# Kernel optimization log

Hardware: AMD Instinct MI355X
Metric: run time of the kernel (lower is better)

## Reference

```python
import jax, jax.numpy as jnp
import numpy as np

N_NODES = 50000
N_EDGES = 800000
DIM = 256
HEADS = 8
DIM_OUT = 32  # per-head; dim_inner = HEADS*DIM_OUT = 256


def setup_inputs() -> dict:
    key = jax.random.key(0)
    ks = jax.random.split(key, 9)
    s = 1.0 / np.sqrt(DIM)
    inner = HEADS * DIM_OUT
    return {
        "x": jax.random.normal(ks[0], (N_NODES, DIM), dtype=jnp.float32),
        "Wq": jax.random.uniform(ks[1], (DIM, inner), jnp.float32, -s, s),
        "bq": jax.random.uniform(ks[2], (inner,), jnp.float32, -s, s),
        "Wk": jax.random.uniform(ks[3], (DIM, inner), jnp.float32, -s, s),
        "bk": jax.random.uniform(ks[4], (inner,), jnp.float32, -s, s),
        "Wv": jax.random.uniform(ks[5], (DIM, inner), jnp.float32, -s, s),
        "bv": jax.random.uniform(ks[6], (inner,), jnp.float32, -s, s),
        "src": jax.random.randint(ks[7], (N_EDGES,), 0, N_NODES),
        "dst": jax.random.randint(ks[8], (N_EDGES,), 0, N_NODES),
    }


def reference(x, Wq, bq, Wk, bk, Wv, bv, src, dst):
    n = x.shape[0]
    q = (x @ Wq + bq).reshape(n, HEADS, DIM_OUT)
    k = (x @ Wk + bk).reshape(n, HEADS, DIM_OUT)
    v = (x @ Wv + bv).reshape(n, HEADS, DIM_OUT)
    # edge-wise u_dot_v: dot of src query with dst key, per head -> [E, H]
    scores = jnp.einsum('ehd,ehd->eh', q[src], k[dst]) / jnp.sqrt(
        jnp.asarray(DIM_OUT, dtype=x.dtype))
    # segment softmax over incoming edges of each destination node
    m = jax.ops.segment_max(scores, dst, num_segments=n)  # [N, H]
    m = jnp.where(jnp.isfinite(m), m, 0.0)
    e = jnp.exp(scores - m[dst])
    z = jax.ops.segment_sum(e, dst, num_segments=n)  # [N, H]
    p = e / jnp.maximum(z[dst], 1e-16)  # [E, H]
    # u_mul_e_sum: sum over incoming edges of src values weighted by attn
    out = jax.ops.segment_sum(v[src] * p[:, :, None], dst, num_segments=n)
    return out.reshape(n, HEADS * DIM_OUT)  # concat=True
```

## Files before the change

kernel.cpp:

```cpp
#include <hip/hip_runtime.h>
#include <math.h>

#define N_NODES 50000
#define N_EDGES 800000
#define DIM 256
#define HEADS 8
#define DIM_OUT 32
#define INNER 256
#define M_PAD 50048

typedef __attribute__((ext_vector_type(8))) short bf16x8;
typedef __attribute__((ext_vector_type(4))) float f32x4;
typedef __attribute__((ext_vector_type(2))) float f32x2;

__device__ __forceinline__ unsigned short f2bf(float f) {
    unsigned u = __float_as_uint(f);
    unsigned r = (u + 0x7FFFu + ((u >> 16) & 1u)) >> 16;
    return (unsigned short)r;
}

__device__ __forceinline__ f32x2 up2(unsigned u) {
    f32x2 r;
    r.x = __uint_as_float(u << 16);
    r.y = __uint_as_float(u & 0xFFFF0000u);
    return r;
}
__device__ __forceinline__ void up2x4(uint4 r, f32x2* o) {
    o[0] = up2(r.x); o[1] = up2(r.y); o[2] = up2(r.z); o[3] = up2(r.w);
}

__device__ __forceinline__ void gll16(const void* g, void* l) {
    __builtin_amdgcn_global_load_lds(
        (const __attribute__((address_space(1))) unsigned*)(uintptr_t)g,
        (__attribute__((address_space(3))) unsigned*)(unsigned)(uintptr_t)l,
        16, 0, 0);
}

#define NB_CONVX 6256
#define NB_CONVW 768
#define NB_HIST  3125
__global__ __launch_bounds__(256) void prep(
    const float* __restrict__ x,
    const float* __restrict__ Wq, const float* __restrict__ Wk,
    const float* __restrict__ Wv,
    const int* __restrict__ dst,
    unsigned short* __restrict__ xbf, unsigned short* __restrict__ Wt,
    int* __restrict__ deg)
{
    int b = blockIdx.x;
    if (b < NB_CONVX) {
        size_t i8 = ((size_t)b * 256 + threadIdx.x) * 8;
        unsigned short h[8];
        if (i8 < (size_t)N_NODES * 256) {
            float4 a = *(const float4*)(x + i8);
            float4 c = *(const float4*)(x + i8 + 4);
            h[0]=f2bf(a.x); h[1]=f2bf(a.y); h[2]=f2bf(a.z); h[3]=f2bf(a.w);
            h[4]=f2bf(c.x); h[5]=f2bf(c.y); h[6]=f2bf(c.z); h[7]=f2bf(c.w);
        } else {
            #pragma unroll
            for (int j = 0; j < 8; j++) h[j] = 0;
        }
        uint4 o;
        o.x = (unsigned)h[0] | ((unsigned)h[1] << 16);
        o.y = (unsigned)h[2] | ((unsigned)h[3] << 16);
        o.z = (unsigned)h[4] | ((unsigned)h[5] << 16);
        o.w = (unsigned)h[6] | ((unsigned)h[7] << 16);
        *(uint4*)(xbf + i8) = o;
    } else if (b < NB_CONVX + NB_CONVW) {
        int idx = (b - NB_CONVX) * 256 + threadIdx.x;
        int z = idx >> 16, r = idx & 65535;
        int k = r >> 8, n = r & 255;
        const float* W = (z == 0) ? Wq : (z == 1) ? Wk : Wv;
        Wt[(size_t)z * 65536 + n * 256 + k] = f2bf(W[k * 256 + n]);
    } else {
        int e = (b - NB_CONVX - NB_CONVW) * 256 + threadIdx.x;
        if (e < N_EDGES) atomicAdd(deg + dst[e], 1);
    }
}

#define GEMM_NWG 2346
__global__ __launch_bounds__(256) void gemm_qkv(
    const unsigned short* __restrict__ xbf,
    const unsigned short* __restrict__ Wt,
    const float* __restrict__ bq, const float* __restrict__ bk,
    const float* __restrict__ bv,
    unsigned short* __restrict__ q, unsigned short* __restrict__ k,
    unsigned short* __restrict__ v)
{
    int hw = blockIdx.x;
    int xcd = hw & 7, pos = hw >> 3;
    const int q8 = GEMM_NWG >> 3, r8 = GEMM_NWG & 7;
    int lid = (xcd < r8 ? xcd * (q8 + 1) : r8 * (q8 + 1) + (xcd - r8) * q8) + pos;
    int xx = lid / 6;
    int yz = lid - xx * 6;
    const int row0 = xx * 128;
    const int col0 = (yz & 1) * 128;
    const int z = yz >> 1;

    const int t = threadIdx.x;
    const unsigned short* Wz = Wt + (size_t)z * 65536;
    const float* bias = (z == 0) ? bq : (z == 1) ? bk : bv;
    unsigned short* C = (z == 0) ? q : (z == 1) ? k : v;

    __shared__ __align__(16) short As[128 * 32];
    __shared__ __align__(16) short Bs[128 * 32];

    const int wave = t >> 6;
    const int lane = t & 63;
    const int wm = (wave & 1) * 64;
    const int wn = (wave >> 1) * 64;
    const int lr = lane & 15;
    const int lg = lane >> 4;
    const int srow = lane >> 2;
    const int sch  = lane & 3;

    f32x4 acc[4][4] = {};

    for (int k0 = 0; k0 < 256; k0 += 32) {
        #pragma unroll
        for (int c = 0; c < 2; c++) {
            int seg = wave * 2 + c;
            gll16(xbf + (size_t)(row0 + seg * 16 + srow) * 256 + k0 + sch * 8,
                  As + seg * 512);
        }
        #pragma unroll
        for (int c = 0; c < 2; c++) {
            int seg = wave * 2 + c;
            gll16(Wz + (size_t)(col0 + seg * 16 + srow) * 256 + k0 + sch * 8,
                  Bs + seg * 512);
        }
        __syncthreads();

        bf16x8 af[4], bfr[4];
        #pragma unroll
        for (int mi = 0; mi < 4; mi++)
            af[mi] = *(const bf16x8*)&As[(wm + mi * 16 + lr) * 32 + lg * 8];
        #pragma unroll
        for (int ni = 0; ni < 4; ni++)
            bfr[ni] = *(const bf16x8*)&Bs[(wn + ni * 16 + lr) * 32 + lg * 8];
        #pragma unroll
        for (int mi = 0; mi < 4; mi++)
            #pragma unroll
            for (int ni = 0; ni < 4; ni++)
                acc[mi][ni] = __builtin_amdgcn_mfma_f32_16x16x32_bf16(
                    af[mi], bfr[ni], acc[mi][ni], 0, 0, 0);
        __syncthreads();
    }

    #pragma unroll
    for (int mi = 0; mi < 4; mi++) {
        #pragma unroll
        for (int ni = 0; ni < 4; ni++) {
            int gcol = col0 + wn + ni * 16 + lr;
            float bb = bias[gcol];
            #pragma unroll
            for (int r = 0; r < 4; r++) {
                int grow = row0 + wm + mi * 16 + lg * 4 + r;
                if (grow < N_NODES)
                    C[(size_t)grow * 256 + gcol] = f2bf(acc[mi][ni][r] + bb);
            }
        }
    }
}

__global__ __launch_bounds__(1024) void scan_deg(
    const int* __restrict__ deg, int* __restrict__ rowptr)
{
    __shared__ int wsum[16];
    __shared__ int wpre[16];
    int t = threadIdx.x;
    int wid = t >> 6, ln = t & 63;
    int carry = 0;
    for (int base = 0; base < N_NODES; base += 4096) {
        int i4 = base + t * 4;
        int4 dv = {0, 0, 0, 0};
        if (i4 < N_NODES) dv = *(const int4*)(deg + i4);
        int sum = dv.x + dv.y + dv.z + dv.w;
        int inc = sum;
        #pragma unroll
        for (int off = 1; off < 64; off <<= 1) {
            int u = __shfl_up(inc, off);
            if (ln >= off) inc += u;
        }
        if (ln == 63) wsum[wid] = inc;
        __syncthreads();
        if (wid == 0 && ln < 16) {
            int s = wsum[ln];
            int p = s;
            #pragma unroll
            for (int off = 1; off < 16; off <<= 1) {
                int u = __shfl_up(p, off);
                if (ln >= off) p += u;
            }
            wpre[ln] = p - s;
        }
        __syncthreads();
        if (i4 < N_NODES) {
            int r = carry + wpre[wid] + (inc - sum);
            r += dv.x; rowptr[i4 + 1] = r;
            r += dv.y; rowptr[i4 + 2] = r;
            r += dv.z; rowptr[i4 + 3] = r;
            r += dv.w; rowptr[i4 + 4] = r;
        }
        carry += wpre[15] + wsum[15];
        __syncthreads();
    }
    if (t == 0) rowptr[0] = 0;
}

__global__ __launch_bounds__(256) void csr_scatter(
    const int* __restrict__ src, const int* __restrict__ dst,
    const int* __restrict__ rowptr,
    int* __restrict__ deg, int* __restrict__ edge_src)
{
    int e = blockIdx.x * 256 + threadIdx.x;
    if (e >= N_EDGES) return;
    int d = dst[e];
    int old = atomicSub(deg + d, 1);
    edge_src[rowptr[d] + old - 1] = src[e];
}

__global__ __launch_bounds__(256) void node_attn(
    const unsigned short* __restrict__ qbf,
    const unsigned short* __restrict__ kbf,
    const unsigned short* __restrict__ vbf,
    const int* __restrict__ rowptr, const int* __restrict__ edge_src,
    float* __restrict__ out)
{
    int node = blockIdx.x * 4 + (threadIdx.x >> 6);
    int lane = threadIdx.x & 63;
    if (node >= N_NODES) return;
    const int half = lane >> 5;
    const int l = lane & 31;

    int beg = rowptr[node], end = rowptr[node + 1];
    int deg = end - beg;

    float* op = out + (size_t)node * 256 + l * 8;
    if (deg <= 0) {
        if (half == 0) {
            float4 z4 = {0.f, 0.f, 0.f, 0.f};
            *(float4*)op = z4;
            *(float4*)(op + 4) = z4;
        }
        return;
    }

    f32x2 kf2[4];
    up2x4(*(const uint4*)(kbf + (size_t)node * 256 + l * 8), kf2);

    const unsigned short* qrow = qbf + l * 8;
    const unsigned short* vrow = vbf + l * 8;

    const float SC = 0.17677669529663687f * 1.4426950408889634f;

    int U = (deg + 1) >> 1;
    U = ((U + 2) / 3) * 3;
    U = __builtin_amdgcn_readfirstlane(U);

    const int i0 = beg + half;
    const int last = end - 1;

    int tmp0 = edge_src[min(i0,     last)];
    int tmp1 = edge_src[min(i0 + 2, last)];
    int idC  = edge_src[min(i0 + 4, last)];
    int idA  = edge_src[min(i0 + 6, last)];
    int idB  = 0;
    uint4 qA = *(const uint4*)(qrow + (size_t)tmp0 * 256);
    uint4 vA = *(const uint4*)(vrow + (size_t)tmp0 * 256);
    uint4 qB = *(const uint4*)(qrow + (size_t)tmp1 * 256);
    uint4 vB = *(const uint4*)(vrow + (size_t)tmp1 * 256);
    uint4 qC, vC;

    float m = -1e30f, zsum = 0.0f;
    f32x2 af2[4] = {};

#define BODY(QW, VW, QL, VL, IDL, IDF, P)                                    \
    do {                                                                     \
        size_t off_ = (size_t)(IDL) * 256;                                   \
        QL = *(const uint4*)(qrow + off_);                                   \
        VL = *(const uint4*)(vrow + off_);                                   \
        int vi_ = i0 + 2 * t + 2 * (P);                                      \
        IDF = edge_src[min(vi_ + 8, last)];                                  \
        f32x2 qf_[4], vf_[4];                                                \
        up2x4(QW, qf_);                                                      \
        up2x4(VW, vf_);                                                      \
        f32x2 d_ = qf_[0] * kf2[0];                                          \
        d_ += qf_[1] * kf2[1];                                               \
        d_ += qf_[2] * kf2[2];                                               \
        d_ += qf_[3] * kf2[3];                                               \
        float s_ = d_.x + d_.y;                                              \
        s_ += __shfl_xor(s_, 1);                                             \
        s_ += __shfl_xor(s_, 2);                                             \
        bool ok_ = vi_ < end;                                                \
        float sc_ = ok_ ? s_ * SC : -1e30f;                                  \
        float mn_ = fmaxf(m, sc_);                                           \
        float w_ = exp2f(sc_ - mn_);                                         \
        w_ = ok_ ? w_ : 0.0f;                                                \
        float al_ = exp2f(m - mn_);                                          \
        zsum = zsum * al_ + w_;                                              \
        f32x2 a2_ = {al_, al_}, w2_ = {w_, w_};                              \
        af2[0] = af2[0] * a2_ + vf_[0] * w2_;                                \
        af2[1] = af2[1] * a2_ + vf_[1] * w2_;                                \
        af2[2] = af2[2] * a2_ + vf_[2] * w2_;                                \
        af2[3] = af2[3] * a2_ + vf_[3] * w2_;                                \
        m = mn_;                                                             \
    } while (0)

    for (int t = 0; t < U; t += 3) {
        BODY(qA, vA, qC, vC, idC, idB, 0);
        BODY(qB, vB, qA, vA, idA, idC, 1);
        BODY(qC, vC, qB, vB, idB, idA, 2);
    }
#undef BODY

    float mo = __shfl_xor(m, 32);
    float mt = fmaxf(m, mo);
    float scale = exp2f(m - mt);
    zsum *= scale;
    zsum += __shfl_xor(zsum, 32);
    #pragma unroll
    for (int j = 0; j < 4; j++) {
        af2[j].x = af2[j].x * scale;
        af2[j].y = af2[j].y * scale;
        af2[j].x += __shfl_xor(af2[j].x, 32);
        af2[j].y += __shfl_xor(af2[j].y, 32);
    }

    float inv = 1.0f / fmaxf(zsum, 1e-16f);
    if (half == 0) {
        float4 o0 = {af2[0].x * inv, af2[0].y * inv, af2[1].x * inv, af2[1].y * inv};
        float4 o1 = {af2[2].x * inv, af2[2].y * inv, af2[3].x * inv, af2[3].y * inv};
        *(float4*)op = o0;
        *(float4*)(op + 4) = o1;
    }
}

extern "C" void kernel_launch(void* const* d_in, const int* in_sizes, int n_in,
                              void* d_out, int out_size, void* d_ws, size_t ws_size,
                              hipStream_t stream) {
    const float* x  = (const float*)d_in[0];
    const float* Wq = (const float*)d_in[1];
    const float* bq = (const float*)d_in[2];
    const float* Wk = (const float*)d_in[3];
    const float* bk = (const float*)d_in[4];
    const float* Wv = (const float*)d_in[5];
    const float* bv = (const float*)d_in[6];
    const int* src  = (const int*)d_in[7];
    const int* dst  = (const int*)d_in[8];
    float* out = (float*)d_out;

    unsigned short* qbf = (unsigned short*)d_ws;
    unsigned short* kbf = qbf + (size_t)N_NODES * INNER;
    unsigned short* vbf = kbf + (size_t)N_NODES * INNER;
    unsigned short* xbf = vbf + (size_t)N_NODES * INNER;
    unsigned short* Wt  = xbf + (size_t)M_PAD * INNER;
    int* deg      = (int*)(Wt + 3 * 65536);
    int* rowptr   = deg + N_NODES;
    int* edge_src = rowptr + (N_NODES + 1);

    hipMemsetAsync(deg, 0, (size_t)N_NODES * sizeof(int), stream);

    prep<<<NB_CONVX + NB_CONVW + NB_HIST, 256, 0, stream>>>(
        x, Wq, Wk, Wv, dst, xbf, Wt, deg);

    gemm_qkv<<<GEMM_NWG, 256, 0, stream>>>(xbf, Wt, bq, bk, bv, qbf, kbf, vbf);

    scan_deg<<<1, 1024, 0, stream>>>(deg, rowptr);
    csr_scatter<<<(N_EDGES + 255) / 256, 256, 0, stream>>>(
        src, dst, rowptr, deg, edge_src);

    node_attn<<<(N_NODES + 3) / 4, 256, 0, stream>>>(
        qbf, kbf, vbf, rowptr, edge_src, out);
}
```

Baseline: 366.6 us.

## Interleave Q and V rows and fold degree scan into GEMM launch

Q and V projections are now written into one interleaved buffer with a 512-element row stride, so each gathered source node's q and v slices sit in adjacent memory and the attention kernel's per-edge loads hit nearby cache lines. The separate single-block prefix-scan kernel is removed and run as one extra 256-thread block inside the GEMM launch, which saves a kernel launch and lets the scan overlap the GEMM. The tradeoffs are a scan with less parallelism (256 threads instead of 1024) that may lengthen the GEMM tail, and strided GEMM stores.

```diff
diff --git a/kernel.cpp b/kernel.cpp
--- a/kernel.cpp
+++ b/kernel.cpp
@@ -84,9 +84,50 @@
     const unsigned short* __restrict__ Wt,
     const float* __restrict__ bq, const float* __restrict__ bk,
     const float* __restrict__ bv,
-    unsigned short* __restrict__ q, unsigned short* __restrict__ k,
-    unsigned short* __restrict__ v)
+    unsigned short* __restrict__ qv, unsigned short* __restrict__ kbf,
+    const int* __restrict__ deg, int* __restrict__ rowptr)
 {
+    const int t = threadIdx.x;
+
+    if (blockIdx.x == GEMM_NWG) {
+        __shared__ int wsum4[4];
+        __shared__ int wpre4[5];
+        int wid = t >> 6, ln = t & 63;
+        int carry = 0;
+        for (int base = 0; base < N_NODES; base += 1024) {
+            int i4 = base + t * 4;
+            int4 dv = {0, 0, 0, 0};
+            if (i4 < N_NODES) dv = *(const int4*)(deg + i4);
+            int sum = dv.x + dv.y + dv.z + dv.w;
+            int inc = sum;
+            #pragma unroll
+            for (int off = 1; off < 64; off <<= 1) {
+                int u = __shfl_up(inc, off);
+                if (ln >= off) inc += u;
+            }
+            if (ln == 63) wsum4[wid] = inc;
+            __syncthreads();
+            if (t == 0) {
+                int a = 0;
+                #pragma unroll
+                for (int j = 0; j < 4; j++) { wpre4[j] = a; a += wsum4[j]; }
+                wpre4[4] = a;
+            }
+            __syncthreads();
+            if (i4 < N_NODES) {
+                int r = carry + wpre4[wid] + (inc - sum);
+                r += dv.x; rowptr[i4 + 1] = r;
+                r += dv.y; rowptr[i4 + 2] = r;
+                r += dv.z; rowptr[i4 + 3] = r;
+                r += dv.w; rowptr[i4 + 4] = r;
+            }
+            carry += wpre4[4];
+            __syncthreads();
+        }
+        if (t == 0) rowptr[0] = 0;
+        return;
+    }
+
     int hw = blockIdx.x;
     int xcd = hw & 7, pos = hw >> 3;
     const int q8 = GEMM_NWG >> 3, r8 = GEMM_NWG & 7;
@@ -97,10 +138,10 @@
     const int col0 = (yz & 1) * 128;
     const int z = yz >> 1;
 
-    const int t = threadIdx.x;
     const unsigned short* Wz = Wt + (size_t)z * 65536;
     const float* bias = (z == 0) ? bq : (z == 1) ? bk : bv;
-    unsigned short* C = (z == 0) ? q : (z == 1) ? k : v;
+    unsigned short* C = (z == 1) ? kbf : (qv + ((z == 0) ? 0 : 256));
+    const int cstride = (z == 1) ? 256 : 512;
 
     __shared__ __align__(16) short As[128 * 32];
     __shared__ __align__(16) short Bs[128 * 32];
@@ -157,55 +198,10 @@
             for (int r = 0; r < 4; r++) {
                 int grow = row0 + wm + mi * 16 + lg * 4 + r;
                 if (grow < N_NODES)
-                    C[(size_t)grow * 256 + gcol] = f2bf(acc[mi][ni][r] + bb);
+                    C[(size_t)grow * cstride + gcol] = f2bf(acc[mi][ni][r] + bb);
             }
         }
     }
-}
-
-__global__ __launch_bounds__(1024) void scan_deg(
-    const int* __restrict__ deg, int* __restrict__ rowptr)
-{
-    __shared__ int wsum[16];
-    __shared__ int wpre[16];
-    int t = threadIdx.x;
-    int wid = t >> 6, ln = t & 63;
-    int carry = 0;
-    for (int base = 0; base < N_NODES; base += 4096) {
-        int i4 = base + t * 4;
-        int4 dv = {0, 0, 0, 0};
-        if (i4 < N_NODES) dv = *(const int4*)(deg + i4);
-        int sum = dv.x + dv.y + dv.z + dv.w;
-        int inc = sum;
-        #pragma unroll
-        for (int off = 1; off < 64; off <<= 1) {
-            int u = __shfl_up(inc, off);
-            if (ln >= off) inc += u;
-        }
-        if (ln == 63) wsum[wid] = inc;
-        __syncthreads();
-        if (wid == 0 && ln < 16) {
-            int s = wsum[ln];
-            int p = s;
-            #pragma unroll
-            for (int off = 1; off < 16; off <<= 1) {
-                int u = __shfl_up(p, off);
-                if (ln >= off) p += u;
-            }
-            wpre[ln] = p - s;
-        }
-        __syncthreads();
-        if (i4 < N_NODES) {
-            int r = carry + wpre[wid] + (inc - sum);
-            r += dv.x; rowptr[i4 + 1] = r;
-            r += dv.y; rowptr[i4 + 2] = r;
-            r += dv.z; rowptr[i4 + 3] = r;
-            r += dv.w; rowptr[i4 + 4] = r;
-        }
-        carry += wpre[15] + wsum[15];
-        __syncthreads();
-    }
-    if (t == 0) rowptr[0] = 0;
 }
 
 __global__ __launch_bounds__(256) void csr_scatter(
@@ -221,9 +217,8 @@
 }
 
 __global__ __launch_bounds__(256) void node_attn(
-    const unsigned short* __restrict__ qbf,
+    const unsigned short* __restrict__ qv,
     const unsigned short* __restrict__ kbf,
-    const unsigned short* __restrict__ vbf,
     const int* __restrict__ rowptr, const int* __restrict__ edge_src,
     float* __restrict__ out)
 {
@@ -249,8 +244,8 @@
     f32x2 kf2[4];
     up2x4(*(const uint4*)(kbf + (size_t)node * 256 + l * 8), kf2);
 
-    const unsigned short* qrow = qbf + l * 8;
-    const unsigned short* vrow = vbf + l * 8;
+    const unsigned short* qrow = qv + l * 8;
+    const unsigned short* vrow = qv + 256 + l * 8;
 
     const float SC = 0.17677669529663687f * 1.4426950408889634f;
 
@@ -266,10 +261,10 @@
     int idC  = edge_src[min(i0 + 4, last)];
     int idA  = edge_src[min(i0 + 6, last)];
     int idB  = 0;
-    uint4 qA = *(const uint4*)(qrow + (size_t)tmp0 * 256);
-    uint4 vA = *(const uint4*)(vrow + (size_t)tmp0 * 256);
-    uint4 qB = *(const uint4*)(qrow + (size_t)tmp1 * 256);
-    uint4 vB = *(const uint4*)(vrow + (size_t)tmp1 * 256);
+    uint4 qA = *(const uint4*)(qrow + (size_t)tmp0 * 512);
+    uint4 vA = *(const uint4*)(vrow + (size_t)tmp0 * 512);
+    uint4 qB = *(const uint4*)(qrow + (size_t)tmp1 * 512);
+    uint4 vB = *(const uint4*)(vrow + (size_t)tmp1 * 512);
     uint4 qC, vC;
 
     float m = -1e30f, zsum = 0.0f;
@@ -277,7 +272,7 @@
 
 #define BODY(QW, VW, QL, VL, IDL, IDF, P)                                    \
     do {                                                                     \
-        size_t off_ = (size_t)(IDL) * 256;                                   \
+        size_t off_ = (size_t)(IDL) * 512;                                   \
         QL = *(const uint4*)(qrow + off_);                                   \
         VL = *(const uint4*)(vrow + off_);                                   \
         int vi_ = i0 + 2 * t + 2 * (P);                                      \
@@ -350,11 +345,10 @@
     const int* dst  = (const int*)d_in[8];
     float* out = (float*)d_out;
 
-    unsigned short* qbf = (unsigned short*)d_ws;
-    unsigned short* kbf = qbf + (size_t)N_NODES * INNER;
-    unsigned short* vbf = kbf + (size_t)N_NODES * INNER;
-    unsigned short* xbf = vbf + (size_t)N_NODES * INNER;
-    unsigned short* Wt  = xbf + (size_t)M_PAD * INNER;
+    unsigned short* qv  = (unsigned short*)d_ws;
+    unsigned short* kbf = qv + (size_t)N_NODES * 512;
+    unsigned short* xbf = kbf + (size_t)N_NODES * 256;
+    unsigned short* Wt  = xbf + (size_t)M_PAD * 256;
     int* deg      = (int*)(Wt + 3 * 65536);
     int* rowptr   = deg + N_NODES;
     int* edge_src = rowptr + (N_NODES + 1);
@@ -364,12 +358,12 @@
     prep<<<NB_CONVX + NB_CONVW + NB_HIST, 256, 0, stream>>>(
         x, Wq, Wk, Wv, dst, xbf, Wt, deg);
 
-    gemm_qkv<<<GEMM_NWG, 256, 0, stream>>>(xbf, Wt, bq, bk, bv, qbf, kbf, vbf);
-
-    scan_deg<<<1, 1024, 0, stream>>>(deg, rowptr);
+    gemm_qkv<<<GEMM_NWG + 1, 256, 0, stream>>>(
+        xbf, Wt, bq, bk, bv, qv, kbf, deg, rowptr);
+
     csr_scatter<<<(N_EDGES + 255) / 256, 256, 0, stream>>>(
         src, dst, rowptr, deg, edge_src);
 
     node_attn<<<(N_NODES + 3) / 4, 256, 0, stream>>>(
-        qbf, kbf, vbf, rowptr, edge_src, out);
-}
+        qv, kbf, rowptr, edge_src, out);
+}
```

After: 377.9 us. 1.03x slower.
